# Performance work log

Hardware: AMD Instinct MI355X
Metric: run time of the kernel (lower is better)

## Reference

```python
import jax, jax.numpy as jnp
import numpy as np

B, S, D = 8, 1024, 768
H, HD = 12, 64  # heads, head dim (H*HD == D)
EPS = 1e-12


def setup_inputs() -> dict:
    key = jax.random.key(0)
    ks = jax.random.split(key, 8)
    s = 0.02
    return {
        "hidden_states": jax.random.normal(ks[0], (B, S, D), jnp.float32),
        "attention_mask": jnp.zeros((B, 1, 1, S), jnp.float32),
        "head_mask": jnp.ones((H,), jnp.float32),
        "Wq": jax.random.normal(ks[1], (D, H * HD), jnp.float32) * s,
        "bq": jnp.zeros((H * HD,), jnp.float32),
        "Wk": jax.random.normal(ks[2], (D, H * HD), jnp.float32) * s,
        "bk": jnp.zeros((H * HD,), jnp.float32),
        "Wv": jax.random.normal(ks[3], (D, H * HD), jnp.float32) * s,
        "bv": jnp.zeros((H * HD,), jnp.float32),
        "Wo": jax.random.normal(ks[4], (D, H * HD), jnp.float32) * s,  # torch Linear weight [out=D, in=H*HD]
        "bo": jnp.zeros((D,), jnp.float32),
        "gamma": jnp.ones((D,), jnp.float32),
        "beta": jnp.zeros((D,), jnp.float32),
    }


def reference(hidden_states, attention_mask, head_mask, Wq, bq, Wk, bk, Wv, bv, Wo, bo, gamma, beta):
    def heads(x):  # [B,S,H*HD] -> [B,H,S,HD]
        return x.reshape(B, S, H, HD).transpose(0, 2, 1, 3)

    q = heads(hidden_states @ Wq.T + bq)
    k = heads(hidden_states @ Wk.T + bk)
    v = heads(hidden_states @ Wv.T + bv)

    scores = jnp.einsum("bhqd,bhkd->bhqk", q, k) / np.sqrt(HD).astype(np.float32)
    scores = scores + attention_mask
    probs = jax.nn.softmax(scores, axis=-1)  # dropout p=0 (eval)
    ctx = jnp.einsum("bhqk,bhkd->bhqd", probs, v)  # [B,H,S,HD]

    # masked per-head output projection: Wo.T.view(H, HD, D)
    Wph = Wo.T.reshape(H, HD, D)
    proj = jnp.einsum("bhsd,hde,h->bse", ctx, Wph, head_mask) + bo

    # residual + LayerNorm
    x = proj + hidden_states
    mu = jnp.mean(x, axis=-1, keepdims=True)
    var = jnp.mean(jnp.square(x - mu), axis=-1, keepdims=True)
    out = (x - mu) * jax.lax.rsqrt(var + EPS) * gamma + beta
    return out
```

## Files before the change

kernel.cpp:

```cpp
#include <hip/hip_runtime.h>
#include <hip/hip_bf16.h>
#include <math.h>

#define Bn 8
#define Sn 1024
#define Dn 768
#define Hn 12
#define MROWS (Bn * Sn)

typedef __attribute__((ext_vector_type(8))) short short8;
typedef __attribute__((ext_vector_type(4))) float floatx4;

__device__ __forceinline__ unsigned short f2b(float x) {
    union { float f; unsigned u; } v; v.f = x;
    unsigned r = v.u + 0x7fffu + ((v.u >> 16) & 1u);
    return (unsigned short)(r >> 16);
}

__device__ __forceinline__ void gload16(const void* g, void* l) {
    __builtin_amdgcn_global_load_lds(
        (const __attribute__((address_space(1))) void*)g,
        (__attribute__((address_space(3))) void*)l, 16, 0, 0);
}

__global__ __launch_bounds__(256) void convert_all(const float* __restrict__ X,
                                                   const float* __restrict__ Wq, const float* __restrict__ Wk,
                                                   const float* __restrict__ Wv, const float* __restrict__ Wo,
                                                   unsigned short* __restrict__ Xb,
                                                   unsigned short* __restrict__ Wqb, unsigned short* __restrict__ Wkb,
                                                   unsigned short* __restrict__ Wvb, unsigned short* __restrict__ Wob) {
    const int id = blockIdx.x;
    const float* src;
    unsigned short* dst;
    int i;
    if (id < 6144) {
        src = X; dst = Xb;
        i = id * 256 + threadIdx.x;
    } else {
        const int y = (id - 6144) / 576;
        src = (y == 0) ? Wq : (y == 1) ? Wk : (y == 2) ? Wv : Wo;
        dst = (y == 0) ? Wqb : (y == 1) ? Wkb : (y == 2) ? Wvb : Wob;
        i = ((id - 6144) % 576) * 256 + threadIdx.x;
    }
    float4 v = reinterpret_cast<const float4*>(src)[i];
    ushort4 o;
    o.x = f2b(v.x); o.y = f2b(v.y); o.z = f2b(v.z); o.w = f2b(v.w);
    reinterpret_cast<ushort4*>(dst)[i] = o;
}

#define QKV_COMPUTE(Ab, Wb)                                                    \
    {                                                                          \
        short8 af[4][2], bf[4][2];                                             \
        _Pragma("unroll") for (int i = 0; i < 4; i++)                          \
            _Pragma("unroll") for (int ks = 0; ks < 2; ks++) {                 \
                af[i][ks] = *(const short8*)&(Ab)[aoff[i][ks]];                \
                bf[i][ks] = *(const short8*)&(Wb)[woff[i][ks]];                \
            }                                                                  \
        _Pragma("unroll") for (int ks = 0; ks < 2; ks++)                       \
            _Pragma("unroll") for (int i = 0; i < 4; i++)                      \
                _Pragma("unroll") for (int j = 0; j < 4; j++)                  \
                    acc[i][j] = __builtin_amdgcn_mfma_f32_16x16x32_bf16(       \
                        af[i][ks], bf[j][ks], acc[i][j], 0, 0, 0);             \
    }

__global__ __launch_bounds__(256) void gemm_qkv(const unsigned short* __restrict__ A,
                                                const unsigned short* __restrict__ Wq,
                                                const unsigned short* __restrict__ Wk,
                                                const unsigned short* __restrict__ Wv,
                                                const float* __restrict__ bq,
                                                const float* __restrict__ bk,
                                                const float* __restrict__ bv,
                                                unsigned short* __restrict__ Qh,
                                                unsigned short* __restrict__ Kh,
                                                unsigned short* __restrict__ Vt) {
    __shared__ __align__(16) unsigned short As[2][128 * 64];
    __shared__ __align__(16) unsigned short Ws[2][128 * 64];
    const int id = blockIdx.x;
    const int by = id & 63;
    const int bx = id >> 6;
    const int mat = bx / 6;
    const int m0 = by * 128;
    const int n0 = (bx % 6) * 128;
    const unsigned short* W = (mat == 0) ? Wq : (mat == 1) ? Wk : Wv;
    const float* bias = (mat == 0) ? bq : (mat == 1) ? bk : bv;
    unsigned short* Cout = (mat == 0) ? Qh : (mat == 1) ? Kh : Vt;

    const int tid = threadIdx.x;
    const int w = tid >> 6, l = tid & 63, quad = l >> 4, mr = l & 15;
    const int wm = (w >> 1) * 64, wn = (w & 1) * 64;

    const unsigned short* gAsrc[4];
    const unsigned short* gWsrc[4];
    unsigned short* lAdst[4];
    unsigned short* lWdst[4];
#pragma unroll
    for (int j = 0; j < 4; j++) {
        const int u = tid + j * 256;
        const int r = u >> 3, c = u & 7;
        const int kq = (c ^ (r & 7)) * 8;
        gAsrc[j] = &A[(size_t)(m0 + r) * Dn + kq];
        gWsrc[j] = &W[(size_t)(n0 + r) * Dn + kq];
        lAdst[j] = &As[0][u * 8];
        lWdst[j] = &Ws[0][u * 8];
    }

    int aoff[4][2], woff[4][2];
#pragma unroll
    for (int i = 0; i < 4; i++) {
        const int ra = wm + i * 16 + mr;
        const int rw = wn + i * 16 + mr;
#pragma unroll
        for (int ks = 0; ks < 2; ks++) {
            aoff[i][ks] = (ra * 8 + ((quad + ks * 4) ^ (ra & 7))) * 8;
            woff[i][ks] = (rw * 8 + ((quad + ks * 4) ^ (rw & 7))) * 8;
        }
    }

    floatx4 acc[4][4];
#pragma unroll
    for (int i = 0; i < 4; i++)
#pragma unroll
        for (int j = 0; j < 4; j++) {
            floatx4 z = {0.f, 0.f, 0.f, 0.f};
            acc[i][j] = z;
        }

    const unsigned short* Af = &As[0][0];
    const unsigned short* Wf = &Ws[0][0];

#pragma unroll
    for (int j = 0; j < 4; j++) {
        gload16(gAsrc[j], lAdst[j]);
        gload16(gWsrc[j], lWdst[j]);
    }
    __syncthreads();

    for (int kt = 0; kt < 12; kt += 2) {
        {
            const int k0 = (kt + 1) * 64;
#pragma unroll
            for (int j = 0; j < 4; j++) {
                gload16(gAsrc[j] + k0, lAdst[j] + 8192);
                gload16(gWsrc[j] + k0, lWdst[j] + 8192);
            }
        }
        QKV_COMPUTE(Af, Wf);
        __syncthreads();

        if (kt + 2 < 12) {
            const int k0 = (kt + 2) * 64;
#pragma unroll
            for (int j = 0; j < 4; j++) {
                gload16(gAsrc[j] + k0, lAdst[j]);
                gload16(gWsrc[j] + k0, lWdst[j]);
            }
        }
        QKV_COMPUTE(Af + 8192, Wf + 8192);
        __syncthreads();
    }

#pragma unroll
    for (int j = 0; j < 4; j++) {
        const int col = n0 + wn + j * 16 + mr;
        const float bval = bias[col];
        const int h = col >> 6, d = col & 63;
#pragma unroll
        for (int i = 0; i < 4; i++) {
            const int mbase = m0 + wm + i * 16 + quad * 4;
            const int b = mbase >> 10, s0 = mbase & 1023;
            const size_t base = (size_t)(b * Hn + h) << 16;
            if (mat == 2) {
                ushort4 o;
                o.x = f2b(acc[i][j][0] + bval);
                o.y = f2b(acc[i][j][1] + bval);
                o.z = f2b(acc[i][j][2] + bval);
                o.w = f2b(acc[i][j][3] + bval);
                *reinterpret_cast<ushort4*>(&Cout[base + (size_t)d * 1024 + s0]) = o;
            } else {
#pragma unroll
                for (int r = 0; r < 4; r++) {
                    const float val = acc[i][j][r] + bval;
                    Cout[base + (size_t)(s0 + r) * 64 + d] = f2b(val);
                }
            }
        }
    }
}

#define OUT_COMPUTE(Ab, Wb)                                                    \
    {                                                                          \
        short8 af[4][2], bf[2][2];                                             \
        _Pragma("unroll") for (int i = 0; i < 4; i++)                          \
            _Pragma("unroll") for (int ks = 0; ks < 2; ks++)                   \
                af[i][ks] = *(const short8*)&(Ab)[aoff[i][ks]];                \
        _Pragma("unroll") for (int j = 0; j < 2; j++)                          \
            _Pragma("unroll") for (int ks = 0; ks < 2; ks++)                   \
                bf[j][ks] = *(const short8*)&(Wb)[woff[j][ks]];                \
        _Pragma("unroll") for (int ks = 0; ks < 2; ks++)                       \
            _Pragma("unroll") for (int i = 0; i < 4; i++)                      \
                _Pragma("unroll") for (int j = 0; j < 2; j++)                  \
                    acc[i][j] = __builtin_amdgcn_mfma_f32_16x16x32_bf16(       \
                        af[i][ks], bf[j][ks], acc[i][j], 0, 0, 0);             \
    }

__global__ __launch_bounds__(256) void gemm_out(const unsigned short* __restrict__ A,
                                                const unsigned short* __restrict__ W,
                                                const float* __restrict__ bias,
                                                const float* __restrict__ X,
                                                float* __restrict__ xres) {
    __shared__ __align__(16) unsigned short As[2][64 * 64];
    __shared__ __align__(16) unsigned short Ws[2][128 * 64];
    const int id = blockIdx.x;
    const int by = id & 127;
    const int bx = id >> 7;
    const int m0 = by * 64;
    const int n0 = bx * 128;

    const int tid = threadIdx.x;
    const int w = tid >> 6, l = tid & 63, quad = l >> 4, mr = l & 15;

    const unsigned short* gAsrc[2];
    unsigned short* lAdst[2];
#pragma unroll
    for (int j = 0; j < 2; j++) {
        const int u = tid + j * 256;
        const int r = u >> 3, c = u & 7;
        gAsrc[j] = &A[(size_t)(m0 + r) * Dn + (c ^ (r & 7)) * 8];
        lAdst[j] = &As[0][u * 8];
    }
    const unsigned short* gWsrc[4];
    unsigned short* lWdst[4];
#pragma unroll
    for (int j = 0; j < 4; j++) {
        const int u = tid + j * 256;
        const int r = u >> 3, c = u & 7;
        gWsrc[j] = &W[(size_t)(n0 + r) * Dn + (c ^ (r & 7)) * 8];
        lWdst[j] = &Ws[0][u * 8];
    }

    int aoff[4][2], woff[2][2];
#pragma unroll
    for (int i = 0; i < 4; i++) {
        const int ra = i * 16 + mr;
#pragma unroll
        for (int ks = 0; ks < 2; ks++)
            aoff[i][ks] = (ra * 8 + ((quad + ks * 4) ^ (ra & 7))) * 8;
    }
#pragma unroll
    for (int j = 0; j < 2; j++) {
        const int rw = w * 32 + j * 16 + mr;
#pragma unroll
        for (int ks = 0; ks < 2; ks++)
            woff[j][ks] = (rw * 8 + ((quad + ks * 4) ^ (rw & 7))) * 8;
    }

    floatx4 acc[4][2];
#pragma unroll
    for (int i = 0; i < 4; i++)
#pragma unroll
        for (int j = 0; j < 2; j++) {
            floatx4 z = {0.f, 0.f, 0.f, 0.f};
            acc[i][j] = z;
        }

    const unsigned short* Af = &As[0][0];
    const unsigned short* Wf = &Ws[0][0];

#pragma unroll
    for (int j = 0; j < 2; j++) gload16(gAsrc[j], lAdst[j]);
#pragma unroll
    for (int j = 0; j < 4; j++) gload16(gWsrc[j], lWdst[j]);
    __syncthreads();

    for (int kt = 0; kt < 12; kt += 2) {
        {
            const int k0 = (kt + 1) * 64;
#pragma unroll
            for (int j = 0; j < 2; j++) gload16(gAsrc[j] + k0, lAdst[j] + 4096);
#pragma unroll
            for (int j = 0; j < 4; j++) gload16(gWsrc[j] + k0, lWdst[j] + 8192);
        }
        OUT_COMPUTE(Af, Wf);
        __syncthreads();

        if (kt + 2 < 12) {
            const int k0 = (kt + 2) * 64;
#pragma unroll
            for (int j = 0; j < 2; j++) gload16(gAsrc[j] + k0, lAdst[j]);
#pragma unroll
            for (int j = 0; j < 4; j++) gload16(gWsrc[j] + k0, lWdst[j]);
        }
        OUT_COMPUTE(Af + 4096, Wf + 8192);
        __syncthreads();
    }

#pragma unroll
    for (int j = 0; j < 2; j++) {
        const int col = n0 + w * 32 + j * 16 + mr;
        const float bval = bias[col];
#pragma unroll
        for (int i = 0; i < 4; i++) {
#pragma unroll
            for (int r = 0; r < 4; r++) {
                const int m = m0 + i * 16 + quad * 4 + r;
                xres[(size_t)m * Dn + col] = acc[i][j][r] + bval + X[(size_t)m * Dn + col];
            }
        }
    }
}

__global__ __launch_bounds__(256) void flash_attn_mfma(const unsigned short* __restrict__ Qh,
                                                       const unsigned short* __restrict__ Kh,
                                                       const unsigned short* __restrict__ Vt,
                                                       const float* __restrict__ mask,
                                                       const float* __restrict__ head_mask,
                                                       unsigned short* __restrict__ ctx) {
    __shared__ __align__(16) unsigned short Ks[64 * 72];
    __shared__ __align__(16) unsigned short Vs[64 * 72];
    __shared__ __align__(16) unsigned short Ps[128 * 72];
    __shared__ float msk[64];

    const int id = blockIdx.x;
    const int bh = id % 96;
    const int qt = id / 96;
    const int b = bh / Hn, h = bh % Hn;
    const int q0 = qt * 128;
    const int tid = threadIdx.x;
    const int w = tid >> 6, l = tid & 63, quad = l >> 4, mr = l & 15;
    const size_t hb = (size_t)(b * Hn + h) << 16;

    short8 aq[2][2];
#pragma unroll
    for (int i = 0; i < 2; i++)
#pragma unroll
        for (int ks = 0; ks < 2; ks++)
            aq[i][ks] = *(const short8*)&Qh[hb + (size_t)(q0 + w * 32 + i * 16 + mr) * 64 + ks * 32 + quad * 8];

    float l_s[2][4];
    floatx4 oacc[2][4];
#pragma unroll
    for (int i = 0; i < 2; i++) {
#pragma unroll
        for (int r = 0; r < 4; r++) l_s[i][r] = 0.f;
#pragma unroll
        for (int jj = 0; jj < 4; jj++) {
            floatx4 z = {0.f, 0.f, 0.f, 0.f};
            oacc[i][jj] = z;
        }
    }

    const int srow = tid >> 2;
    const int scol = (tid & 3) * 16;

    short8 pk0 = *(const short8*)&Kh[hb + (size_t)srow * 64 + scol];
    short8 pk1 = *(const short8*)&Kh[hb + (size_t)srow * 64 + scol + 8];
    short8 pv0 = *(const short8*)&Vt[hb + (size_t)srow * 1024 + scol];
    short8 pv1 = *(const short8*)&Vt[hb + (size_t)srow * 1024 + scol + 8];
    float pm = mask[b * Sn + (tid & 63)];

    for (int kt = 0; kt < Sn / 64; kt++) {
        __syncthreads();
        *(short8*)&Ks[srow * 72 + scol] = pk0;
        *(short8*)&Ks[srow * 72 + scol + 8] = pk1;
        *(short8*)&Vs[srow * 72 + scol] = pv0;
        *(short8*)&Vs[srow * 72 + scol + 8] = pv1;
        if (tid < 64) msk[tid] = pm;
        if (kt < Sn / 64 - 1) {
            const int k0 = (kt + 1) * 64;
            pk0 = *(const short8*)&Kh[hb + (size_t)(k0 + srow) * 64 + scol];
            pk1 = *(const short8*)&Kh[hb + (size_t)(k0 + srow) * 64 + scol + 8];
            pv0 = *(const short8*)&Vt[hb + (size_t)srow * 1024 + k0 + scol];
            pv1 = *(const short8*)&Vt[hb + (size_t)srow * 1024 + k0 + scol + 8];
            pm = mask[b * Sn + k0 + (tid & 63)];
        }
        __syncthreads();

        floatx4 sacc[2][4];
#pragma unroll
        for (int i = 0; i < 2; i++)
#pragma unroll
            for (int j = 0; j < 4; j++) {
                floatx4 z = {0.f, 0.f, 0.f, 0.f};
                sacc[i][j] = z;
            }
#pragma unroll
        for (int ks = 0; ks < 2; ks++) {
#pragma unroll
            for (int j = 0; j < 4; j++) {
                short8 bk = *(const short8*)&Ks[(j * 16 + mr) * 72 + ks * 32 + quad * 8];
                sacc[0][j] = __builtin_amdgcn_mfma_f32_16x16x32_bf16(aq[0][ks], bk, sacc[0][j], 0, 0, 0);
                sacc[1][j] = __builtin_amdgcn_mfma_f32_16x16x32_bf16(aq[1][ks], bk, sacc[1][j], 0, 0, 0);
            }
        }

#pragma unroll
        for (int i = 0; i < 2; i++) {
#pragma unroll
            for (int j = 0; j < 4; j++) {
                const float mk = msk[j * 16 + mr];
#pragma unroll
                for (int r = 0; r < 4; r++) {
                    const float p = __expf(sacc[i][j][r] * 0.125f + mk);
                    l_s[i][r] += p;
                    Ps[(w * 32 + i * 16 + quad * 4 + r) * 72 + j * 16 + mr] = f2b(p);
                }
            }
        }

#pragma unroll
        for (int ks = 0; ks < 2; ks++) {
            short8 ap0 = *(const short8*)&Ps[(w * 32 + mr) * 72 + ks * 32 + quad * 8];
            short8 ap1 = *(const short8*)&Ps[(w * 32 + 16 + mr) * 72 + ks * 32 + quad * 8];
#pragma unroll
            for (int jj = 0; jj < 4; jj++) {
                short8 bv = *(const short8*)&Vs[(jj * 16 + mr) * 72 + ks * 32 + quad * 8];
                oacc[0][jj] = __builtin_amdgcn_mfma_f32_16x16x32_bf16(ap0, bv, oacc[0][jj], 0, 0, 0);
                oacc[1][jj] = __builtin_amdgcn_mfma_f32_16x16x32_bf16(ap1, bv, oacc[1][jj], 0, 0, 0);
            }
        }
    }

    const float hm = head_mask[h];
    float inv[2][4];
#pragma unroll
    for (int i = 0; i < 2; i++)
#pragma unroll
        for (int r = 0; r < 4; r++) {
            float t = l_s[i][r];
            t += __shfl_xor(t, 1);
            t += __shfl_xor(t, 2);
            t += __shfl_xor(t, 4);
            t += __shfl_xor(t, 8);
            inv[i][r] = hm / t;
        }
#pragma unroll
    for (int i = 0; i < 2; i++)
#pragma unroll
        for (int jj = 0; jj < 4; jj++)
#pragma unroll
            for (int r = 0; r < 4; r++) {
                const int qrow = q0 + w * 32 + i * 16 + quad * 4 + r;
                ctx[(size_t)(b * Sn + qrow) * Dn + h * 64 + jj * 16 + mr] = f2b(oacc[i][jj][r] * inv[i][r]);
            }
}

__global__ __launch_bounds__(256) void ln_kernel(const float* __restrict__ x,
                                                 const float* __restrict__ gamma,
                                                 const float* __restrict__ beta,
                                                 float* __restrict__ out) {
    __shared__ float r1[4];
    __shared__ float r2[4];
    const int m = blockIdx.x;
    const int tid = threadIdx.x;
    const int w = tid >> 6, lane = tid & 63;

    float xv[3];
    float s = 0.f, ss = 0.f;
#pragma unroll
    for (int i = 0; i < 3; i++) {
        int j = tid + i * 256;
        float t = x[(size_t)m * Dn + j];
        xv[i] = t;
        s += t;
        ss += t * t;
    }
#pragma unroll
    for (int o = 1; o < 64; o <<= 1) {
        s += __shfl_xor(s, o);
        ss += __shfl_xor(ss, o);
    }
    if (lane == 0) { r1[w] = s; r2[w] = ss; }
    __syncthreads();
    const float sum = r1[0] + r1[1] + r1[2] + r1[3];
    const float sqs = r2[0] + r2[1] + r2[2] + r2[3];
    const float mu = sum * (1.0f / Dn);
    const float var = sqs * (1.0f / Dn) - mu * mu;
    const float rstd = rsqrtf(var + 1e-12f);
#pragma unroll
    for (int i = 0; i < 3; i++) {
        int j = tid + i * 256;
        out[(size_t)m * Dn + j] = (xv[i] - mu) * rstd * gamma[j] + beta[j];
    }
}

extern "C" void kernel_launch(void* const* d_in, const int* in_sizes, int n_in,
                              void* d_out, int out_size, void* d_ws, size_t ws_size,
                              hipStream_t stream) {
    const float* X         = (const float*)d_in[0];
    const float* mask      = (const float*)d_in[1];
    const float* head_mask = (const float*)d_in[2];
    const float* Wq        = (const float*)d_in[3];
    const float* bq        = (const float*)d_in[4];
    const float* Wk        = (const float*)d_in[5];
    const float* bk        = (const float*)d_in[6];
    const float* Wv        = (const float*)d_in[7];
    const float* bv        = (const float*)d_in[8];
    const float* Wo        = (const float*)d_in[9];
    const float* bo        = (const float*)d_in[10];
    const float* gamma     = (const float*)d_in[11];
    const float* beta      = (const float*)d_in[12];
    float* out = (float*)d_out;

    const size_t NE = (size_t)Bn * Sn * Dn;
    const size_t NW = (size_t)Dn * Dn;

    char* p = (char*)d_ws;
    unsigned short* Xb  = (unsigned short*)p;  p += NE * 2;
    unsigned short* Wqb = (unsigned short*)p;  p += NW * 2;
    unsigned short* Wkb = (unsigned short*)p;  p += NW * 2;
    unsigned short* Wvb = (unsigned short*)p;  p += NW * 2;
    unsigned short* Wob = (unsigned short*)p;  p += NW * 2;
    unsigned short* Qh  = (unsigned short*)p;  p += NE * 2;
    unsigned short* Kh  = (unsigned short*)p;  p += NE * 2;
    unsigned short* Vtb = (unsigned short*)p;  p += NE * 2;
    unsigned short* ctx = (unsigned short*)p;  p += NE * 2;
    float* xres = (float*)p;

    convert_all<<<8448, 256, 0, stream>>>(X, Wq, Wk, Wv, Wo, Xb, Wqb, Wkb, Wvb, Wob);

    gemm_qkv<<<1152, 256, 0, stream>>>(Xb, Wqb, Wkb, Wvb, bq, bk, bv, Qh, Kh, Vtb);

    flash_attn_mfma<<<768, 256, 0, stream>>>(Qh, Kh, Vtb, mask, head_mask, ctx);

    gemm_out<<<768, 256, 0, stream>>>(ctx, Wob, bo, X, xres);

    ln_kernel<<<MROWS, 256, 0, stream>>>(xres, gamma, beta, out);
}
```

Measured before the change: 223.8 us.

## Use fine-grained vmcnt waits, setprio around MFMA, and transposed QK^T with exp2 softmax

The GEMM kernels replace __syncthreads with explicit s_waitcnt vmcnt(N) plus raw barriers, so the load into the next buffer can stay in flight while the current tile is computed. MFMA blocks are wrapped in s_setprio to favour the matrix issue. The attention kernel computes S^T (K as the A operand), folds the 1/sqrt(d) scale and log2e into a single exp2, packs bf16 pairs for vectorized P stores, and simplifies the row-sum reduction. This relies on correct vmcnt counts; a wrong count could race on LDS.

```diff
diff --git a/kernel.cpp b/kernel.cpp
--- a/kernel.cpp
+++ b/kernel.cpp
@@ -17,11 +17,29 @@
     return (unsigned short)(r >> 16);
 }
 
+__device__ __forceinline__ unsigned pk2(float a, float b) {
+    union { __hip_bfloat162 h; unsigned u; } v;
+    v.h = __float22bfloat162_rn(float2{a, b});
+    return v.u;
+}
+
+__device__ __forceinline__ float fexp2(float x) {
+    float r;
+    asm("v_exp_f32 %0, %1" : "=v"(r) : "v"(x));
+    return r;
+}
+
 __device__ __forceinline__ void gload16(const void* g, void* l) {
     __builtin_amdgcn_global_load_lds(
         (const __attribute__((address_space(1))) void*)g,
         (__attribute__((address_space(3))) void*)l, 16, 0, 0);
 }
+
+#define MEMFENCE() asm volatile("" ::: "memory")
+#define WAITV8()  asm volatile("s_waitcnt vmcnt(8)" ::: "memory")
+#define WAITV6()  asm volatile("s_waitcnt vmcnt(6)" ::: "memory")
+#define WAITV0()  asm volatile("s_waitcnt vmcnt(0)" ::: "memory")
+#define WAITLGKM() asm volatile("s_waitcnt lgkmcnt(0)" ::: "memory")
 
 __global__ __launch_bounds__(256) void convert_all(const float* __restrict__ X,
                                                    const float* __restrict__ Wq, const float* __restrict__ Wk,
@@ -56,11 +74,13 @@
                 af[i][ks] = *(const short8*)&(Ab)[aoff[i][ks]];                \
                 bf[i][ks] = *(const short8*)&(Wb)[woff[i][ks]];                \
             }                                                                  \
+        __builtin_amdgcn_s_setprio(1);                                         \
         _Pragma("unroll") for (int ks = 0; ks < 2; ks++)                       \
             _Pragma("unroll") for (int i = 0; i < 4; i++)                      \
                 _Pragma("unroll") for (int j = 0; j < 4; j++)                  \
                     acc[i][j] = __builtin_amdgcn_mfma_f32_16x16x32_bf16(       \
                         af[i][ks], bf[j][ks], acc[i][j], 0, 0, 0);             \
+        __builtin_amdgcn_s_setprio(0);                                         \
     }
 
 __global__ __launch_bounds__(256) void gemm_qkv(const unsigned short* __restrict__ A,
@@ -133,7 +153,6 @@
         gload16(gAsrc[j], lAdst[j]);
         gload16(gWsrc[j], lWdst[j]);
     }
-    __syncthreads();
 
     for (int kt = 0; kt < 12; kt += 2) {
         {
@@ -144,8 +163,12 @@
                 gload16(gWsrc[j] + k0, lWdst[j] + 8192);
             }
         }
+        WAITV8();
+        __builtin_amdgcn_s_barrier();
+        MEMFENCE();
         QKV_COMPUTE(Af, Wf);
-        __syncthreads();
+        __builtin_amdgcn_s_barrier();
+        MEMFENCE();
 
         if (kt + 2 < 12) {
             const int k0 = (kt + 2) * 64;
@@ -154,9 +177,15 @@
                 gload16(gAsrc[j] + k0, lAdst[j]);
                 gload16(gWsrc[j] + k0, lWdst[j]);
             }
-        }
+            WAITV8();
+        } else {
+            WAITV0();
+        }
+        __builtin_amdgcn_s_barrier();
+        MEMFENCE();
         QKV_COMPUTE(Af + 8192, Wf + 8192);
-        __syncthreads();
+        __builtin_amdgcn_s_barrier();
+        MEMFENCE();
     }
 
 #pragma unroll
@@ -196,11 +225,13 @@
         _Pragma("unroll") for (int j = 0; j < 2; j++)                          \
             _Pragma("unroll") for (int ks = 0; ks < 2; ks++)                   \
                 bf[j][ks] = *(const short8*)&(Wb)[woff[j][ks]];                \
+        __builtin_amdgcn_s_setprio(1);                                         \
         _Pragma("unroll") for (int ks = 0; ks < 2; ks++)                       \
             _Pragma("unroll") for (int i = 0; i < 4; i++)                      \
                 _Pragma("unroll") for (int j = 0; j < 2; j++)                  \
                     acc[i][j] = __builtin_amdgcn_mfma_f32_16x16x32_bf16(       \
                         af[i][ks], bf[j][ks], acc[i][j], 0, 0, 0);             \
+        __builtin_amdgcn_s_setprio(0);                                         \
     }
 
 __global__ __launch_bounds__(256) void gemm_out(const unsigned short* __restrict__ A,
@@ -270,7 +301,6 @@
     for (int j = 0; j < 2; j++) gload16(gAsrc[j], lAdst[j]);
 #pragma unroll
     for (int j = 0; j < 4; j++) gload16(gWsrc[j], lWdst[j]);
-    __syncthreads();
 
     for (int kt = 0; kt < 12; kt += 2) {
         {
@@ -280,8 +310,12 @@
 #pragma unroll
             for (int j = 0; j < 4; j++) gload16(gWsrc[j] + k0, lWdst[j] + 8192);
         }
+        WAITV6();
+        __builtin_amdgcn_s_barrier();
+        MEMFENCE();
         OUT_COMPUTE(Af, Wf);
-        __syncthreads();
+        __builtin_amdgcn_s_barrier();
+        MEMFENCE();
 
         if (kt + 2 < 12) {
             const int k0 = (kt + 2) * 64;
@@ -289,9 +323,15 @@
             for (int j = 0; j < 2; j++) gload16(gAsrc[j] + k0, lAdst[j]);
 #pragma unroll
             for (int j = 0; j < 4; j++) gload16(gWsrc[j] + k0, lWdst[j]);
-        }
+            WAITV6();
+        } else {
+            WAITV0();
+        }
+        __builtin_amdgcn_s_barrier();
+        MEMFENCE();
         OUT_COMPUTE(Af + 4096, Wf + 8192);
-        __syncthreads();
+        __builtin_amdgcn_s_barrier();
+        MEMFENCE();
     }
 
 #pragma unroll
@@ -320,6 +360,9 @@
     __shared__ __align__(16) unsigned short Ps[128 * 72];
     __shared__ float msk[64];
 
+    const float LOG2E = 1.44269504088896f;
+    const float C1 = 0.125f * 1.44269504088896f;
+
     const int id = blockIdx.x;
     const int bh = id % 96;
     const int qt = id / 96;
@@ -331,23 +374,20 @@
 
     short8 aq[2][2];
 #pragma unroll
+    for (int j = 0; j < 2; j++)
+#pragma unroll
+        for (int ks = 0; ks < 2; ks++)
+            aq[j][ks] = *(const short8*)&Qh[hb + (size_t)(q0 + w * 32 + j * 16 + mr) * 64 + ks * 32 + quad * 8];
+
+    float l_s[2] = {0.f, 0.f};
+    floatx4 oacc[2][4];
+#pragma unroll
     for (int i = 0; i < 2; i++)
-#pragma unroll
-        for (int ks = 0; ks < 2; ks++)
-            aq[i][ks] = *(const short8*)&Qh[hb + (size_t)(q0 + w * 32 + i * 16 + mr) * 64 + ks * 32 + quad * 8];
-
-    float l_s[2][4];
-    floatx4 oacc[2][4];
-#pragma unroll
-    for (int i = 0; i < 2; i++) {
-#pragma unroll
-        for (int r = 0; r < 4; r++) l_s[i][r] = 0.f;
 #pragma unroll
         for (int jj = 0; jj < 4; jj++) {
             floatx4 z = {0.f, 0.f, 0.f, 0.f};
             oacc[i][jj] = z;
         }
-    }
 
     const int srow = tid >> 2;
     const int scol = (tid & 3) * 16;
@@ -359,12 +399,13 @@
     float pm = mask[b * Sn + (tid & 63)];
 
     for (int kt = 0; kt < Sn / 64; kt++) {
-        __syncthreads();
+        __builtin_amdgcn_s_barrier();
+        MEMFENCE();
         *(short8*)&Ks[srow * 72 + scol] = pk0;
         *(short8*)&Ks[srow * 72 + scol + 8] = pk1;
         *(short8*)&Vs[srow * 72 + scol] = pv0;
         *(short8*)&Vs[srow * 72 + scol + 8] = pv1;
-        if (tid < 64) msk[tid] = pm;
+        if (tid < 64) msk[tid] = pm * LOG2E;
         if (kt < Sn / 64 - 1) {
             const int k0 = (kt + 1) * 64;
             pk0 = *(const short8*)&Kh[hb + (size_t)(k0 + srow) * 64 + scol];
@@ -373,37 +414,48 @@
             pv1 = *(const short8*)&Vt[hb + (size_t)srow * 1024 + k0 + scol + 8];
             pm = mask[b * Sn + k0 + (tid & 63)];
         }
-        __syncthreads();
-
-        floatx4 sacc[2][4];
-#pragma unroll
-        for (int i = 0; i < 2; i++)
-#pragma unroll
-            for (int j = 0; j < 4; j++) {
+        WAITLGKM();
+        __builtin_amdgcn_s_barrier();
+        MEMFENCE();
+
+        floatx4 sacc[4][2];
+#pragma unroll
+        for (int i = 0; i < 4; i++)
+#pragma unroll
+            for (int j = 0; j < 2; j++) {
                 floatx4 z = {0.f, 0.f, 0.f, 0.f};
                 sacc[i][j] = z;
             }
 #pragma unroll
         for (int ks = 0; ks < 2; ks++) {
-#pragma unroll
-            for (int j = 0; j < 4; j++) {
-                short8 bk = *(const short8*)&Ks[(j * 16 + mr) * 72 + ks * 32 + quad * 8];
-                sacc[0][j] = __builtin_amdgcn_mfma_f32_16x16x32_bf16(aq[0][ks], bk, sacc[0][j], 0, 0, 0);
-                sacc[1][j] = __builtin_amdgcn_mfma_f32_16x16x32_bf16(aq[1][ks], bk, sacc[1][j], 0, 0, 0);
-            }
-        }
-
-#pragma unroll
-        for (int i = 0; i < 2; i++) {
-#pragma unroll
-            for (int j = 0; j < 4; j++) {
-                const float mk = msk[j * 16 + mr];
+            short8 kfr[4];
+#pragma unroll
+            for (int i = 0; i < 4; i++)
+                kfr[i] = *(const short8*)&Ks[(i * 16 + mr) * 72 + ks * 32 + quad * 8];
+            __builtin_amdgcn_s_setprio(1);
+#pragma unroll
+            for (int i = 0; i < 4; i++)
+#pragma unroll
+                for (int j = 0; j < 2; j++)
+                    sacc[i][j] = __builtin_amdgcn_mfma_f32_16x16x32_bf16(kfr[i], aq[j][ks], sacc[i][j], 0, 0, 0);
+            __builtin_amdgcn_s_setprio(0);
+        }
+
+#pragma unroll
+        for (int i = 0; i < 4; i++) {
+            floatx4 mk4 = *(const floatx4*)&msk[i * 16 + quad * 4];
+#pragma unroll
+            for (int j = 0; j < 2; j++) {
+                float p[4];
 #pragma unroll
                 for (int r = 0; r < 4; r++) {
-                    const float p = __expf(sacc[i][j][r] * 0.125f + mk);
-                    l_s[i][r] += p;
-                    Ps[(w * 32 + i * 16 + quad * 4 + r) * 72 + j * 16 + mr] = f2b(p);
+                    p[r] = fexp2(sacc[i][j][r] * C1 + mk4[r]);
+                    l_s[j] += p[r];
                 }
+                uint2 w2;
+                w2.x = pk2(p[0], p[1]);
+                w2.y = pk2(p[2], p[3]);
+                *(uint2*)&Ps[(w * 32 + j * 16 + mr) * 72 + i * 16 + quad * 4] = w2;
             }
         }
 
@@ -411,28 +463,33 @@
         for (int ks = 0; ks < 2; ks++) {
             short8 ap0 = *(const short8*)&Ps[(w * 32 + mr) * 72 + ks * 32 + quad * 8];
             short8 ap1 = *(const short8*)&Ps[(w * 32 + 16 + mr) * 72 + ks * 32 + quad * 8];
+            __builtin_amdgcn_s_setprio(1);
 #pragma unroll
             for (int jj = 0; jj < 4; jj++) {
                 short8 bv = *(const short8*)&Vs[(jj * 16 + mr) * 72 + ks * 32 + quad * 8];
                 oacc[0][jj] = __builtin_amdgcn_mfma_f32_16x16x32_bf16(ap0, bv, oacc[0][jj], 0, 0, 0);
                 oacc[1][jj] = __builtin_amdgcn_mfma_f32_16x16x32_bf16(ap1, bv, oacc[1][jj], 0, 0, 0);
             }
-        }
-    }
-
+            __builtin_amdgcn_s_setprio(0);
+        }
+    }
+
+    float L[2];
+#pragma unroll
+    for (int j = 0; j < 2; j++) {
+        float t = l_s[j];
+        t += __shfl_xor(t, 16);
+        t += __shfl_xor(t, 32);
+        L[j] = t;
+    }
     const float hm = head_mask[h];
     float inv[2][4];
 #pragma unroll
     for (int i = 0; i < 2; i++)
 #pragma unroll
-        for (int r = 0; r < 4; r++) {
-            float t = l_s[i][r];
-            t += __shfl_xor(t, 1);
-            t += __shfl_xor(t, 2);
-            t += __shfl_xor(t, 4);
-            t += __shfl_xor(t, 8);
-            inv[i][r] = hm / t;
-        }
+        for (int r = 0; r < 4; r++)
+            inv[i][r] = hm / __shfl(L[i], quad * 4 + r);
+
 #pragma unroll
     for (int i = 0; i < 2; i++)
 #pragma unroll
```

Result: faster. 213.2 us (-4.7%).
